# Performance work log

Measured on AMD Instinct MI355X. Metric: run time of the kernel, lower is better.

The kernel has to match this reference:

```python
import jax, jax.numpy as jnp
import numpy as np

M, N, D, P = 16, 2048, 128, 8192
H = N // D  # 16
MAXLEN = 8448
EPS = 1e-5


def layernorm(x, g, b):
    mu = jnp.mean(x, axis=-1, keepdims=True)
    var = jnp.mean(jnp.square(x - mu), axis=-1, keepdims=True)
    return (x - mu) * jax.lax.rsqrt(var + EPS) * g + b


def setup_inputs() -> dict:
    key = jax.random.key(0)
    ks = jax.random.split(key, 10)
    s = 1.0 / np.sqrt(N)  # keep activations O(1) like trained weights
    return {
        "X": jax.random.normal(ks[0], (M, N), jnp.float32),
        "ln1_g": jnp.ones((N,), jnp.float32),
        "ln1_b": jnp.zeros((N,), jnp.float32),
        "Wq": jax.random.normal(ks[1], (N, N), jnp.float32) * s,
        "Wk": jax.random.normal(ks[2], (N, N), jnp.float32) * s,
        "Wv": jax.random.normal(ks[3], (N, N), jnp.float32) * s,
        "Wo": jax.random.normal(ks[4], (N, N), jnp.float32) * s,
        "ln2_g": jnp.ones((N,), jnp.float32),
        "ln2_b": jnp.zeros((N,), jnp.float32),
        "Wup": jax.random.normal(ks[5], (4 * N, N), jnp.float32) * s,
        "Wdown": jax.random.normal(ks[6], (N, 4 * N), jnp.float32) * (1.0 / np.sqrt(4 * N)),
        "cache_K": jax.random.normal(ks[7], (H, MAXLEN, D), jnp.float32),
        "cache_V": jax.random.normal(ks[8], (H, MAXLEN, D), jnp.float32),
    }


def reference(X, ln1_g, ln1_b, Wq, Wk, Wv, Wo, ln2_g, ln2_b, Wup, Wdown, cache_K, cache_V):
    residual = X
    Xn = layernorm(X, ln1_g, ln1_b)
    # torch Linear: y = x @ W.T
    q = (Xn @ Wq.T).reshape(M, H, D).transpose(1, 0, 2)  # (H,M,D)
    k = (Xn @ Wk.T).reshape(M, H, D).transpose(1, 0, 2)
    v = (Xn @ Wv.T).reshape(M, H, D).transpose(1, 0, 2)
    # KV-cache append
    cache_K = jax.lax.dynamic_update_slice(cache_K, k, (0, P, 0))
    cache_V = jax.lax.dynamic_update_slice(cache_V, v, (0, P, 0))
    Kc = cache_K[:, : P + M, :]  # (H,T,D), T = P+M
    Vc = cache_V[:, : P + M, :]
    scores = jnp.einsum("hmd,htd->hmt", q, Kc) / np.sqrt(D)
    weights = jax.nn.softmax(scores, axis=-1)
    attn = jnp.einsum("hmt,htd->hmd", weights, Vc)  # (H,M,D)
    attn = attn.transpose(1, 0, 2).reshape(M, N)
    X = residual + attn @ Wo.T
    residual = X
    Xn = layernorm(X, ln2_g, ln2_b)
    ffn = jax.nn.gelu(Xn @ Wup.T, approximate=False) @ Wdown.T
    return residual + ffn
```

## Files before the change

### kernel.cpp

```cpp
#include <hip/hip_runtime.h>
#include <hip/hip_bf16.h>
#include <math.h>

#define M_TOK 16
#define NDIM  2048
#define DHEAD 128
#define NHEAD 16
#define MAXLEN 8448
#define FFN   8192
#define TC    64
#define NCH   129
#define LN_EPS 1e-5f
#define RSQRT_D 0.08838834764831845f

#define AS1 __attribute__((address_space(1)))
#define AS3 __attribute__((address_space(3)))

typedef float f4v __attribute__((ext_vector_type(4)));
typedef float f2v __attribute__((ext_vector_type(2)));
typedef short bf16x8 __attribute__((ext_vector_type(8)));

__device__ __forceinline__ void gload_lds16(const float* g, float* l) {
    __builtin_amdgcn_global_load_lds((AS1 void*)g, (AS3 void*)l, 16, 0, 0);
}

__device__ __forceinline__ uint32_t lds_off(const void* p) {
    return (uint32_t)(uintptr_t)(const AS3 void*)p;
}

__device__ __forceinline__ f4v dsr_b128(uint32_t off) {
    f4v r; asm volatile("ds_read_b128 %0, %1" : "=v"(r) : "v"(off)); return r;
}
__device__ __forceinline__ float dsr_b32(uint32_t off) {
    float r; asm volatile("ds_read_b32 %0, %1" : "=v"(r) : "v"(off)); return r;
}
__device__ __forceinline__ void dsw_b32(uint32_t off, float v) {
    asm volatile("ds_write_b32 %0, %1" : : "v"(off), "v"(v));
}
__device__ __forceinline__ f4v gload_b128(const float* p) {
    f4v r;
    asm volatile("global_load_dwordx4 %0, %1, off"
                 : "=v"(r) : "v"((unsigned long long)(uintptr_t)p));
    return r;
}
#define LGKM0()  asm volatile("s_waitcnt lgkmcnt(0)" ::: "memory")
#define VM0()    asm volatile("s_waitcnt vmcnt(0)" ::: "memory")
#define SCHED0() __builtin_amdgcn_sched_barrier(0)

__device__ __forceinline__ short f2bf(float x) {
    unsigned u = __float_as_uint(x);
    unsigned r = u + 0x7fffu + ((u >> 16) & 1u);
    return (short)(r >> 16);
}

template<int H>
__device__ __forceinline__ void fold_step(float* v, int lane, int o) {
    bool hi = (lane & o) != 0;
    #pragma unroll
    for (int i = 0; i < H; ++i) {
        float send = hi ? v[i] : v[i + H];
        float keep = hi ? v[i + H] : v[i];
        v[i] = keep + __shfl_xor(send, o);
    }
}

__device__ __forceinline__ void fold32(float* v, int lane) {
    fold_step<16>(v, lane, 32);
    fold_step<8>(v, lane, 16);
    fold_step<4>(v, lane, 8);
    fold_step<2>(v, lane, 4);
    fold_step<1>(v, lane, 2);
    v[0] += __shfl_xor(v[0], 1);
}

template<int KDIM>
__device__ __forceinline__ void gemv_core8(const float* __restrict__ A,
                                           const float* __restrict__ W,
                                           int cb, int w, int lane,
                                           float* sbuf, float* acc) {
    constexpr int NS = KDIM / 256;
    const float* wsrc0 = W + (size_t)(cb + 2 * w)     * KDIM + lane * 4;
    const float* wsrc1 = W + (size_t)(cb + 2 * w + 1) * KDIM + lane * 4;
    auto issue = [&](int s) {
        if (s >= NS) return;
        float* dst = sbuf + (s % 3) * 6144;
        gload_lds16(wsrc0 + s * 256, dst + (2 * w) * 256);
        gload_lds16(wsrc1 + s * 256, dst + (2 * w + 1) * 256);
        #pragma unroll
        for (int j = 0; j < 4; ++j) {
            int m = w * 4 + j;
            gload_lds16(A + (size_t)m * KDIM + s * 256 + lane * 4,
                        dst + 2048 + m * 256);
        }
    };
    issue(0); issue(1); issue(2);
    const uint32_t sb = lds_off(sbuf);
    #pragma unroll 1
    for (int s = 0; s < NS; ++s) {
        int rem = NS - 1 - s;
        if (rem >= 2)      asm volatile("s_waitcnt vmcnt(12)" ::: "memory");
        else if (rem == 1) asm volatile("s_waitcnt vmcnt(6)" ::: "memory");
        else               asm volatile("s_waitcnt vmcnt(0)" ::: "memory");
        __builtin_amdgcn_s_barrier();
        SCHED0();
        uint32_t b = sb + (uint32_t)((s % 3) * 6144) * 4u;
        f4v wr0 = dsr_b128(b + (uint32_t)((2 * w) * 256 + lane * 4) * 4u);
        f4v wr1 = dsr_b128(b + (uint32_t)((2 * w + 1) * 256 + lane * 4) * 4u);
        f4v xr[16];
        #pragma unroll
        for (int m = 0; m < 16; ++m)
            xr[m] = dsr_b128(b + (uint32_t)(2048 + m * 256 + lane * 4) * 4u);
        LGKM0();
        SCHED0();
        __builtin_amdgcn_s_barrier();
        issue(s + 3);
        #pragma unroll
        for (int m = 0; m < 16; ++m) {
            acc[m*2]   = fmaf(wr0.x, xr[m].x, acc[m*2]);
            acc[m*2]   = fmaf(wr0.y, xr[m].y, acc[m*2]);
            acc[m*2]   = fmaf(wr0.z, xr[m].z, acc[m*2]);
            acc[m*2]   = fmaf(wr0.w, xr[m].w, acc[m*2]);
            acc[m*2+1] = fmaf(wr1.x, xr[m].x, acc[m*2+1]);
            acc[m*2+1] = fmaf(wr1.y, xr[m].y, acc[m*2+1]);
            acc[m*2+1] = fmaf(wr1.z, xr[m].z, acc[m*2+1]);
            acc[m*2+1] = fmaf(wr1.w, xr[m].w, acc[m*2+1]);
        }
    }
}

__global__ __launch_bounds__(256) void k_qkv(const float* __restrict__ Xn,
                                             const float* __restrict__ Wq,
                                             const float* __restrict__ Wk,
                                             const float* __restrict__ Wv,
                                             float* __restrict__ qws,
                                             float* __restrict__ kws,
                                             float* __restrict__ vws) {
    __shared__ float sbuf[3 * 6144];
    int tid = threadIdx.x, w = tid >> 6, lane = tid & 63;
    int b = blockIdx.x;
    int sel = b >> 8;
    int cb = (b & 255) * 8;
    const float* W = (sel == 0) ? Wq : (sel == 1) ? Wk : Wv;
    float* dst = (sel == 0) ? qws : (sel == 1) ? kws : vws;
    float acc[32];
    #pragma unroll
    for (int i = 0; i < 32; ++i) acc[i] = 0.f;
    gemv_core8<2048>(Xn, W, cb, w, lane, sbuf, acc);
    fold32(acc, lane);
    if ((lane & 1) == 0) {
        int idx = (lane >> 1) & 31;
        int m = idx >> 1, c = idx & 1;
        int gcol = cb + 2 * w + c;
        int hh = gcol >> 7, d = gcol & 127;
        dst[(((size_t)hh * 16 + m) << 7) + d] = acc[0];
    }
}

__device__ __forceinline__ float gelu_exact(float x) {
    return 0.5f * x * (1.0f + erff(x * 0.7071067811865475f));
}

__global__ __launch_bounds__(256) void k_up(const float* __restrict__ A,
                                            const float* __restrict__ W,
                                            float* __restrict__ out) {
    __shared__ float sbuf[3 * 6144];
    int tid = threadIdx.x, w = tid >> 6, lane = tid & 63;
    int cb = blockIdx.x * 8;
    float acc[32];
    #pragma unroll
    for (int i = 0; i < 32; ++i) acc[i] = 0.f;
    gemv_core8<2048>(A, W, cb, w, lane, sbuf, acc);
    fold32(acc, lane);
    if ((lane & 1) == 0) {
        int idx = (lane >> 1) & 31;
        int m = idx >> 1, c = idx & 1;
        out[(size_t)m * FFN + cb + 2 * w + c] = gelu_exact(acc[0]);
    }
}

template<int KDIM>
__global__ __launch_bounds__(256) void k_resid(const float* __restrict__ A,
                                               const float* __restrict__ W,
                                               const float* __restrict__ R,
                                               float* __restrict__ out) {
    __shared__ float sbuf[3 * 6144];
    int tid = threadIdx.x, w = tid >> 6, lane = tid & 63;
    int cb = blockIdx.x * 8;
    float acc[32];
    #pragma unroll
    for (int i = 0; i < 32; ++i) acc[i] = 0.f;
    gemv_core8<KDIM>(A, W, cb, w, lane, sbuf, acc);
    fold32(acc, lane);
    if ((lane & 1) == 0) {
        int idx = (lane >> 1) & 31;
        int m = idx >> 1, c = idx & 1;
        int col = cb + 2 * w + c;
        out[(size_t)m * NDIM + col] = R[(size_t)m * NDIM + col] + acc[0];
    }
}

__global__ __launch_bounds__(256) void k_ln(const float* __restrict__ X,
                                            const float* __restrict__ g,
                                            const float* __restrict__ b,
                                            float* __restrict__ out) {
    int row = blockIdx.x, tid = threadIdx.x;
    const float4* xp = (const float4*)(X + (size_t)row * NDIM);
    float4 v0 = xp[tid], v1 = xp[tid + 256];
    float s = v0.x + v0.y + v0.z + v0.w + v1.x + v1.y + v1.z + v1.w;
    float q = v0.x*v0.x + v0.y*v0.y + v0.z*v0.z + v0.w*v0.w
            + v1.x*v1.x + v1.y*v1.y + v1.z*v1.z + v1.w*v1.w;
    #pragma unroll
    for (int o = 32; o; o >>= 1) { s += __shfl_xor(s, o); q += __shfl_xor(q, o); }
    __shared__ float ls[4], lq[4];
    int wid = tid >> 6, lane = tid & 63;
    if (lane == 0) { ls[wid] = s; lq[wid] = q; }
    __syncthreads();
    s = ls[0] + ls[1] + ls[2] + ls[3];
    q = lq[0] + lq[1] + lq[2] + lq[3];
    float mu  = s * (1.f / NDIM);
    float var = q * (1.f / NDIM) - mu * mu;
    float rs  = rsqrtf(var + LN_EPS);
    float4 g0 = ((const float4*)g)[tid], g1 = ((const float4*)g)[tid + 256];
    float4 b0 = ((const float4*)b)[tid], b1 = ((const float4*)b)[tid + 256];
    float4 o0, o1;
    o0.x = (v0.x - mu) * rs * g0.x + b0.x;  o0.y = (v0.y - mu) * rs * g0.y + b0.y;
    o0.z = (v0.z - mu) * rs * g0.z + b0.z;  o0.w = (v0.w - mu) * rs * g0.w + b0.w;
    o1.x = (v1.x - mu) * rs * g1.x + b1.x;  o1.y = (v1.y - mu) * rs * g1.y + b1.y;
    o1.z = (v1.z - mu) * rs * g1.z + b1.z;  o1.w = (v1.w - mu) * rs * g1.w + b1.w;
    float4* op = (float4*)(out + (size_t)row * NDIM);
    op[tid] = o0; op[tid + 256] = o1;
}

__global__ __launch_bounds__(256) void k_attn(const float* __restrict__ cacheK,
                                              const float* __restrict__ cacheV,
                                              const float* __restrict__ qws,
                                              const float* __restrict__ kws,
                                              const float* __restrict__ vws,
                                              float* __restrict__ part,
                                              float* __restrict__ ms) {
    __shared__ float s_k[TC * DHEAD];
    __shared__ float s_v[TC * DHEAD];
    __shared__ float s_p[16 * 68];
    int bid = blockIdx.x;
    int h = bid / NCH, c = bid % NCH;
    int nT = (c < NCH - 1) ? TC : M_TOK;
    bool full = (nT == TC);
    int nSeg = nT >> 1;
    const float* Kb = (c < NCH - 1) ? cacheK + ((size_t)h * MAXLEN + (size_t)c * TC) * DHEAD
                                    : kws + (size_t)h * M_TOK * DHEAD;
    const float* Vb = (c < NCH - 1) ? cacheV + ((size_t)h * MAXLEN + (size_t)c * TC) * DHEAD
                                    : vws + (size_t)h * M_TOK * DHEAD;
    int tid = threadIdx.x, w = tid >> 6, lane = tid & 63;
    int g = lane >> 4;

    #pragma unroll
    for (int k = 0; k < 8; ++k) {
        int j = w + 4 * k;
        if (j < nSeg) {
            int b = j * 1024 + lane * 16;
            int src = b ^ (((b >> 9) & 7) << 4);
            gload_lds16(Kb + (src >> 2), s_k + j * 256);
        }
    }

    int m_l = lane & 15;
    const float* qbase = qws + (size_t)h * M_TOK * DHEAD + (size_t)m_l * DHEAD;
    f4v qlo[4], qhi[4];
    #pragma unroll
    for (int blk = 0; blk < 4; ++blk) {
        qlo[blk] = gload_b128(qbase + blk * 32 + g * 4);
        qhi[blk] = gload_b128(qbase + blk * 32 + g * 4 + 16);
    }
    VM0();
    SCHED0();

    bf16x8 qf[4];
    #pragma unroll
    for (int blk = 0; blk < 4; ++blk) {
        qf[blk][0] = f2bf(qlo[blk].x); qf[blk][1] = f2bf(qlo[blk].y);
        qf[blk][2] = f2bf(qlo[blk].z); qf[blk][3] = f2bf(qlo[blk].w);
        qf[blk][4] = f2bf(qhi[blk].x); qf[blk][5] = f2bf(qhi[blk].y);
        qf[blk][6] = f2bf(qhi[blk].z); qf[blk][7] = f2bf(qhi[blk].w);
    }

    #pragma unroll
    for (int k = 0; k < 8; ++k) {
        int j = w + 4 * k;
        if (j < nSeg) {
            int b = j * 1024 + lane * 16;
            int src = b ^ (((b >> 9) & 7) << 4);
            gload_lds16(Vb + (src >> 2), s_v + j * 256);
        }
    }
    __builtin_amdgcn_s_barrier();

    const uint32_t skb = lds_off(s_k);
    const uint32_t svb = lds_off(s_v);
    const uint32_t spb = lds_off(s_p);

    int t0 = w * 16;
    if (t0 < nT) {
        int trow = t0 + (lane & 15);
        uint32_t xo = (uint32_t)((trow & 7) << 4);
        f4v klo[4], khi[4];
        #pragma unroll
        for (int blk = 0; blk < 4; ++blk) {
            uint32_t base = (uint32_t)(trow * 512 + blk * 128 + g * 16);
            klo[blk] = dsr_b128(skb + ((base)      ^ xo));
            khi[blk] = dsr_b128(skb + ((base + 64) ^ xo));
        }
        LGKM0();
        SCHED0();
        f4v accS = {0.f, 0.f, 0.f, 0.f};
        #pragma unroll
        for (int blk = 0; blk < 4; ++blk) {
            bf16x8 bk;
            bk[0] = f2bf(klo[blk].x); bk[1] = f2bf(klo[blk].y);
            bk[2] = f2bf(klo[blk].z); bk[3] = f2bf(klo[blk].w);
            bk[4] = f2bf(khi[blk].x); bk[5] = f2bf(khi[blk].y);
            bk[6] = f2bf(khi[blk].z); bk[7] = f2bf(khi[blk].w);
            accS = __builtin_amdgcn_mfma_f32_16x16x32_bf16(qf[blk], bk, accS, 0, 0, 0);
        }
        #pragma unroll
        for (int r = 0; r < 4; ++r) {
            int m = g * 4 + r;
            dsw_b32(spb + (uint32_t)((m * 68 + t0 + (lane & 15)) * 4), accS[r] * RSQRT_D);
        }
    }
    LGKM0();
    __builtin_amdgcn_s_barrier();

    int m2 = tid >> 4, tl = tid & 15;
    float sm_mx, sm_sum;
    {
        uint32_t prow = spb + (uint32_t)(m2 * 68 * 4);
        float r0 = dsr_b32(prow + (uint32_t)(tl * 4));
        float r1 = -1e30f, r2 = -1e30f, r3 = -1e30f;
        if (full) {
            r1 = dsr_b32(prow + (uint32_t)((tl + 16) * 4));
            r2 = dsr_b32(prow + (uint32_t)((tl + 32) * 4));
            r3 = dsr_b32(prow + (uint32_t)((tl + 48) * 4));
        }
        LGKM0();
        SCHED0();
        float mx = fmaxf(fmaxf(r0, r1), fmaxf(r2, r3));
        #pragma unroll
        for (int o = 8; o; o >>= 1) mx = fmaxf(mx, __shfl_xor(mx, o));
        float p0 = __expf(r0 - mx), sum = p0;
        dsw_b32(prow + (uint32_t)(tl * 4), p0);
        if (full) {
            float p1 = __expf(r1 - mx), p2 = __expf(r2 - mx), p3 = __expf(r3 - mx);
            sum += p1 + p2 + p3;
            dsw_b32(prow + (uint32_t)((tl + 16) * 4), p1);
            dsw_b32(prow + (uint32_t)((tl + 32) * 4), p2);
            dsw_b32(prow + (uint32_t)((tl + 48) * 4), p3);
        }
        #pragma unroll
        for (int o = 8; o; o >>= 1) sum += __shfl_xor(sum, o);
        sm_mx = mx; sm_sum = sum;
    }
    LGKM0();
    VM0();
    __builtin_amdgcn_s_barrier();

    if (!full) {
        for (int i = tid; i < 16 * 128; i += 256) {
            int r = 16 + (i >> 7), dd = i & 127;
            dsw_b32(svb + (uint32_t)((r * 512 + dd * 4) ^ ((r & 7) << 4)), 0.f);
        }
        { int m = tid >> 4, t = 16 + (tid & 15);
          dsw_b32(spb + (uint32_t)((m * 68 + t) * 4), 0.f); }
        LGKM0();
        __builtin_amdgcn_s_barrier();
    }

    f4v accO0 = {0.f,0.f,0.f,0.f}, accO1 = {0.f,0.f,0.f,0.f};
    int dc0 = w * 32 + (lane & 15);
    int nTC = (nT + 31) >> 5;
    #pragma unroll
    for (int tc = 0; tc < 2; ++tc) {
        if (tc >= nTC) break;
        int m = lane & 15;
        f4v plo = dsr_b128(spb + (uint32_t)((m * 68 + tc * 32 + g * 4) * 4));
        f4v phi = dsr_b128(spb + (uint32_t)((m * 68 + tc * 32 + g * 4 + 16) * 4));
        float va[8], vb_[8];
        #pragma unroll
        for (int half = 0; half < 2; ++half) {
            #pragma unroll
            for (int jj = 0; jj < 4; ++jj) {
                int t = tc * 32 + g * 4 + jj + half * 16;
                uint32_t xo = (uint32_t)((t & 7) << 4);
                va[half*4+jj]  = dsr_b32(svb + ((uint32_t)(t * 512 + dc0 * 4)        ^ xo));
                vb_[half*4+jj] = dsr_b32(svb + ((uint32_t)(t * 512 + (dc0+16) * 4)   ^ xo));
            }
        }
        LGKM0();
        SCHED0();
        bf16x8 pa;
        pa[0] = f2bf(plo.x); pa[1] = f2bf(plo.y); pa[2] = f2bf(plo.z); pa[3] = f2bf(plo.w);
        pa[4] = f2bf(phi.x); pa[5] = f2bf(phi.y); pa[6] = f2bf(phi.z); pa[7] = f2bf(phi.w);
        bf16x8 v0, v1;
        #pragma unroll
        for (int j = 0; j < 8; ++j) { v0[j] = f2bf(va[j]); v1[j] = f2bf(vb_[j]); }
        accO0 = __builtin_amdgcn_mfma_f32_16x16x32_bf16(pa, v0, accO0, 0, 0, 0);
        accO1 = __builtin_amdgcn_mfma_f32_16x16x32_bf16(pa, v1, accO1, 0, 0, 0);
    }

    float* pb = part + ((size_t)(h * NCH + c) * 16) * DHEAD;
    #pragma unroll
    for (int r = 0; r < 4; ++r) {
        int m = g * 4 + r;
        pb[(size_t)m * DHEAD + dc0]      = accO0[r];
        pb[(size_t)m * DHEAD + dc0 + 16] = accO1[r];
    }
    if (tl == 0) {
        float* msp = ms + ((size_t)(h * NCH + c) * 16 + m2) * 2;
        msp[0] = sm_mx; msp[1] = sm_sum;
    }
}

__global__ __launch_bounds__(256) void k_combine(const float* __restrict__ part,
                                                 const float* __restrict__ ms,
                                                 float* __restrict__ attnout) {
    __shared__ float s_scale[16][NCH + 3];
    int h = blockIdx.x >> 3, dblk = blockIdx.x & 7;
    int tid = threadIdx.x;
    {
        int cl = tid & 15, m = tid >> 4;
        float gmax = -1e30f;
        for (int c = cl; c < NCH; c += 16)
            gmax = fmaxf(gmax, ms[((size_t)(h * NCH + c) * 16 + m) * 2]);
        #pragma unroll
        for (int o = 8; o; o >>= 1) gmax = fmaxf(gmax, __shfl_xor(gmax, o));
        float denom = 0.f;
        for (int c = cl; c < NCH; c += 16) {
            const float* msp = ms + ((size_t)(h * NCH + c) * 16 + m) * 2;
            denom += msp[1] * __expf(msp[0] - gmax);
        }
        #pragma unroll
        for (int o = 8; o; o >>= 1) denom += __shfl_xor(denom, o);
        float inv = 1.f / denom;
        for (int c = cl; c < NCH; c += 16) {
            const float* msp = ms + ((size_t)(h * NCH + c) * 16 + m) * 2;
            s_scale[m][c] = __expf(msp[0] - gmax) * inv;
        }
    }
    __syncthreads();
    int m = tid >> 4, dd = tid & 15;
    int d = dblk * 16 + dd;
    const float* pp = part + ((size_t)h * NCH * 16 + m) * DHEAD + d;
    float acc = 0.f;
    #pragma unroll 4
    for (int c = 0; c < NCH; ++c)
        acc = fmaf(pp[(size_t)c * 16 * DHEAD], s_scale[m][c], acc);
    attnout[(size_t)m * NDIM + h * DHEAD + d] = acc;
}

extern "C" void kernel_launch(void* const* d_in, const int* in_sizes, int n_in,
                              void* d_out, int out_size, void* d_ws, size_t ws_size,
                              hipStream_t stream) {
    const float* X      = (const float*)d_in[0];
    const float* ln1_g  = (const float*)d_in[1];
    const float* ln1_b  = (const float*)d_in[2];
    const float* Wq     = (const float*)d_in[3];
    const float* Wk     = (const float*)d_in[4];
    const float* Wv     = (const float*)d_in[5];
    const float* Wo     = (const float*)d_in[6];
    const float* ln2_g  = (const float*)d_in[7];
    const float* ln2_b  = (const float*)d_in[8];
    const float* Wup    = (const float*)d_in[9];
    const float* Wdown  = (const float*)d_in[10];
    const float* cacheK = (const float*)d_in[11];
    const float* cacheV = (const float*)d_in[12];
    float* out = (float*)d_out;

    float* ws = (float*)d_ws;
    float* Xn1    = ws;
    float* qws    = Xn1 + 32768;
    float* kws    = qws + 32768;
    float* vws    = kws + 32768;
    float* partb  = vws + 32768;
    float* msb    = partb + 4227072;
    float* attn_o = msb + 66048;
    float* X2     = attn_o + 32768;
    float* Xn2    = X2 + 32768;
    float* ffnh   = Xn2 + 32768;

    k_ln<<<M_TOK, 256, 0, stream>>>(X, ln1_g, ln1_b, Xn1);
    k_qkv<<<768, 256, 0, stream>>>(Xn1, Wq, Wk, Wv, qws, kws, vws);
    k_attn<<<NHEAD * NCH, 256, 0, stream>>>(cacheK, cacheV, qws, kws, vws, partb, msb);
    k_combine<<<NHEAD * 8, 256, 0, stream>>>(partb, msb, attn_o);
    k_resid<2048><<<256, 256, 0, stream>>>(attn_o, Wo, X, X2);
    k_ln<<<M_TOK, 256, 0, stream>>>(X2, ln2_g, ln2_b, Xn2);
    k_up<<<1024, 256, 0, stream>>>(Xn2, Wup, ffnh);
    k_resid<8192><<<256, 256, 0, stream>>>(ffnh, Wdown, X2, out);
}
```

Before: 141.8 us.

## Replace FP32 LDS-staged GEMVs with split-K bf16 MFMA GEMMs plus epilogue kernels

```diff
diff --git a/kernel.cpp b/kernel.cpp
--- a/kernel.cpp
+++ b/kernel.cpp
@@ -23,11 +23,9 @@
 __device__ __forceinline__ void gload_lds16(const float* g, float* l) {
     __builtin_amdgcn_global_load_lds((AS1 void*)g, (AS3 void*)l, 16, 0, 0);
 }
-
 __device__ __forceinline__ uint32_t lds_off(const void* p) {
     return (uint32_t)(uintptr_t)(const AS3 void*)p;
 }
-
 __device__ __forceinline__ f4v dsr_b128(uint32_t off) {
     f4v r; asm volatile("ds_read_b128 %0, %1" : "=v"(r) : "v"(off)); return r;
 }
@@ -43,6 +41,13 @@
                  : "=v"(r) : "v"((unsigned long long)(uintptr_t)p));
     return r;
 }
+template<int OFF>
+__device__ __forceinline__ f4v gload_off(const float* p) {
+    f4v r;
+    asm volatile("global_load_dwordx4 %0, %1, off offset:%2"
+                 : "=v"(r) : "v"((unsigned long long)(uintptr_t)p), "i"(OFF));
+    return r;
+}
 #define LGKM0()  asm volatile("s_waitcnt lgkmcnt(0)" ::: "memory")
 #define VM0()    asm volatile("s_waitcnt vmcnt(0)" ::: "memory")
 #define SCHED0() __builtin_amdgcn_sched_barrier(0)
@@ -52,151 +57,130 @@
     unsigned r = u + 0x7fffu + ((u >> 16) & 1u);
     return (short)(r >> 16);
 }
-
-template<int H>
-__device__ __forceinline__ void fold_step(float* v, int lane, int o) {
-    bool hi = (lane & o) != 0;
-    #pragma unroll
-    for (int i = 0; i < H; ++i) {
-        float send = hi ? v[i] : v[i + H];
-        float keep = hi ? v[i + H] : v[i];
-        v[i] = keep + __shfl_xor(send, o);
-    }
-}
-
-__device__ __forceinline__ void fold32(float* v, int lane) {
-    fold_step<16>(v, lane, 32);
-    fold_step<8>(v, lane, 16);
-    fold_step<4>(v, lane, 8);
-    fold_step<2>(v, lane, 4);
-    fold_step<1>(v, lane, 2);
-    v[0] += __shfl_xor(v[0], 1);
-}
-
-template<int KDIM>
-__device__ __forceinline__ void gemv_core8(const float* __restrict__ A,
-                                           const float* __restrict__ W,
-                                           int cb, int w, int lane,
-                                           float* sbuf, float* acc) {
-    constexpr int NS = KDIM / 256;
-    const float* wsrc0 = W + (size_t)(cb + 2 * w)     * KDIM + lane * 4;
-    const float* wsrc1 = W + (size_t)(cb + 2 * w + 1) * KDIM + lane * 4;
-    auto issue = [&](int s) {
-        if (s >= NS) return;
-        float* dst = sbuf + (s % 3) * 6144;
-        gload_lds16(wsrc0 + s * 256, dst + (2 * w) * 256);
-        gload_lds16(wsrc1 + s * 256, dst + (2 * w + 1) * 256);
-        #pragma unroll
-        for (int j = 0; j < 4; ++j) {
-            int m = w * 4 + j;
-            gload_lds16(A + (size_t)m * KDIM + s * 256 + lane * 4,
-                        dst + 2048 + m * 256);
-        }
-    };
-    issue(0); issue(1); issue(2);
-    const uint32_t sb = lds_off(sbuf);
-    #pragma unroll 1
-    for (int s = 0; s < NS; ++s) {
-        int rem = NS - 1 - s;
-        if (rem >= 2)      asm volatile("s_waitcnt vmcnt(12)" ::: "memory");
-        else if (rem == 1) asm volatile("s_waitcnt vmcnt(6)" ::: "memory");
-        else               asm volatile("s_waitcnt vmcnt(0)" ::: "memory");
-        __builtin_amdgcn_s_barrier();
-        SCHED0();
-        uint32_t b = sb + (uint32_t)((s % 3) * 6144) * 4u;
-        f4v wr0 = dsr_b128(b + (uint32_t)((2 * w) * 256 + lane * 4) * 4u);
-        f4v wr1 = dsr_b128(b + (uint32_t)((2 * w + 1) * 256 + lane * 4) * 4u);
-        f4v xr[16];
-        #pragma unroll
-        for (int m = 0; m < 16; ++m)
-            xr[m] = dsr_b128(b + (uint32_t)(2048 + m * 256 + lane * 4) * 4u);
-        LGKM0();
-        SCHED0();
-        __builtin_amdgcn_s_barrier();
-        issue(s + 3);
-        #pragma unroll
-        for (int m = 0; m < 16; ++m) {
-            acc[m*2]   = fmaf(wr0.x, xr[m].x, acc[m*2]);
-            acc[m*2]   = fmaf(wr0.y, xr[m].y, acc[m*2]);
-            acc[m*2]   = fmaf(wr0.z, xr[m].z, acc[m*2]);
-            acc[m*2]   = fmaf(wr0.w, xr[m].w, acc[m*2]);
-            acc[m*2+1] = fmaf(wr1.x, xr[m].x, acc[m*2+1]);
-            acc[m*2+1] = fmaf(wr1.y, xr[m].y, acc[m*2+1]);
-            acc[m*2+1] = fmaf(wr1.z, xr[m].z, acc[m*2+1]);
-            acc[m*2+1] = fmaf(wr1.w, xr[m].w, acc[m*2+1]);
-        }
-    }
-}
-
-__global__ __launch_bounds__(256) void k_qkv(const float* __restrict__ Xn,
-                                             const float* __restrict__ Wq,
-                                             const float* __restrict__ Wk,
-                                             const float* __restrict__ Wv,
-                                             float* __restrict__ qws,
-                                             float* __restrict__ kws,
-                                             float* __restrict__ vws) {
-    __shared__ float sbuf[3 * 6144];
+__device__ __forceinline__ bf16x8 to8(f4v lo, f4v hi) {
+    bf16x8 r;
+    r[0]=f2bf(lo.x); r[1]=f2bf(lo.y); r[2]=f2bf(lo.z); r[3]=f2bf(lo.w);
+    r[4]=f2bf(hi.x); r[5]=f2bf(hi.y); r[6]=f2bf(hi.z); r[7]=f2bf(hi.w);
+    return r;
+}
+
+__device__ __forceinline__ f4v gemm16_512(const float* a, const float* wp) {
+    f4v acc = {0.f, 0.f, 0.f, 0.f};
+    f4v al[4][2], bl[4][2];
+#define ISSUE(c) \
+    al[(c)&3][0] = gload_off<(c)*128>(a);      \
+    al[(c)&3][1] = gload_off<(c)*128+16>(a);   \
+    bl[(c)&3][0] = gload_off<(c)*128>(wp);     \
+    bl[(c)&3][1] = gload_off<(c)*128+16>(wp);
+#define STEP(c) { \
+    if ((c) <= 12)      asm volatile("s_waitcnt vmcnt(12)" ::: "memory"); \
+    else if ((c) == 13) asm volatile("s_waitcnt vmcnt(8)"  ::: "memory"); \
+    else if ((c) == 14) asm volatile("s_waitcnt vmcnt(4)"  ::: "memory"); \
+    else                asm volatile("s_waitcnt vmcnt(0)"  ::: "memory"); \
+    SCHED0(); \
+    { bf16x8 af = to8(al[(c)&3][0], al[(c)&3][1]); \
+      bf16x8 bf = to8(bl[(c)&3][0], bl[(c)&3][1]); \
+      acc = __builtin_amdgcn_mfma_f32_16x16x32_bf16(af, bf, acc, 0, 0, 0); } \
+    if ((c) + 4 < 16) { ISSUE((c)+4) } }
+    ISSUE(0) ISSUE(1) ISSUE(2) ISSUE(3)
+    STEP(0)  STEP(1)  STEP(2)  STEP(3)
+    STEP(4)  STEP(5)  STEP(6)  STEP(7)
+    STEP(8)  STEP(9)  STEP(10) STEP(11)
+    STEP(12) STEP(13) STEP(14) STEP(15)
+#undef STEP
+#undef ISSUE
+    return acc;
+}
+
+template<int K, int N, int S>
+__global__ __launch_bounds__(256) void k_mm(const float* __restrict__ A,
+                                            const float* __restrict__ W,
+                                            float* __restrict__ part) {
+    int tid = threadIdx.x, w = tid >> 6, lane = tid & 63;
+    int nColBlk = N >> 6;
+    int colblk = blockIdx.x % nColBlk, s = blockIdx.x / nColBlk;
+    int cb = colblk * 64 + w * 16;
+    int col = cb + (lane & 15), g = lane >> 4, k0 = s * 512;
+    f4v acc = gemm16_512(A + (size_t)(lane & 15) * K + k0 + g * 8,
+                         W + (size_t)col * K + k0 + g * 8);
+    #pragma unroll
+    for (int r = 0; r < 4; ++r)
+        part[((size_t)(s * 16) + g * 4 + r) * N + col] = acc[r];
+}
+
+__global__ __launch_bounds__(256) void k_qkv_mm(const float* __restrict__ Xn,
+                                                const float* __restrict__ Wq,
+                                                const float* __restrict__ Wk,
+                                                const float* __restrict__ Wv,
+                                                float* __restrict__ pq,
+                                                float* __restrict__ pk,
+                                                float* __restrict__ pv) {
     int tid = threadIdx.x, w = tid >> 6, lane = tid & 63;
     int b = blockIdx.x;
-    int sel = b >> 8;
-    int cb = (b & 255) * 8;
+    int sel = b >> 7, bb = b & 127;
+    int colblk = bb & 31, s = bb >> 5;
     const float* W = (sel == 0) ? Wq : (sel == 1) ? Wk : Wv;
-    float* dst = (sel == 0) ? qws : (sel == 1) ? kws : vws;
-    float acc[32];
-    #pragma unroll
-    for (int i = 0; i < 32; ++i) acc[i] = 0.f;
-    gemv_core8<2048>(Xn, W, cb, w, lane, sbuf, acc);
-    fold32(acc, lane);
-    if ((lane & 1) == 0) {
-        int idx = (lane >> 1) & 31;
-        int m = idx >> 1, c = idx & 1;
-        int gcol = cb + 2 * w + c;
-        int hh = gcol >> 7, d = gcol & 127;
-        dst[(((size_t)hh * 16 + m) << 7) + d] = acc[0];
-    }
+    float* part = (sel == 0) ? pq : (sel == 1) ? pk : pv;
+    int cb = colblk * 64 + w * 16;
+    int col = cb + (lane & 15), g = lane >> 4, k0 = s * 512;
+    f4v acc = gemm16_512(Xn + (size_t)(lane & 15) * NDIM + k0 + g * 8,
+                         W + (size_t)col * NDIM + k0 + g * 8);
+    #pragma unroll
+    for (int r = 0; r < 4; ++r)
+        part[((size_t)(s * 16) + g * 4 + r) * NDIM + col] = acc[r];
 }
 
 __device__ __forceinline__ float gelu_exact(float x) {
     return 0.5f * x * (1.0f + erff(x * 0.7071067811865475f));
 }
 
-__global__ __launch_bounds__(256) void k_up(const float* __restrict__ A,
-                                            const float* __restrict__ W,
-                                            float* __restrict__ out) {
-    __shared__ float sbuf[3 * 6144];
-    int tid = threadIdx.x, w = tid >> 6, lane = tid & 63;
-    int cb = blockIdx.x * 8;
-    float acc[32];
-    #pragma unroll
-    for (int i = 0; i < 32; ++i) acc[i] = 0.f;
-    gemv_core8<2048>(A, W, cb, w, lane, sbuf, acc);
-    fold32(acc, lane);
-    if ((lane & 1) == 0) {
-        int idx = (lane >> 1) & 31;
-        int m = idx >> 1, c = idx & 1;
-        out[(size_t)m * FFN + cb + 2 * w + c] = gelu_exact(acc[0]);
-    }
-}
-
-template<int KDIM>
-__global__ __launch_bounds__(256) void k_resid(const float* __restrict__ A,
-                                               const float* __restrict__ W,
-                                               const float* __restrict__ R,
-                                               float* __restrict__ out) {
-    __shared__ float sbuf[3 * 6144];
-    int tid = threadIdx.x, w = tid >> 6, lane = tid & 63;
-    int cb = blockIdx.x * 8;
-    float acc[32];
-    #pragma unroll
-    for (int i = 0; i < 32; ++i) acc[i] = 0.f;
-    gemv_core8<KDIM>(A, W, cb, w, lane, sbuf, acc);
-    fold32(acc, lane);
-    if ((lane & 1) == 0) {
-        int idx = (lane >> 1) & 31;
-        int m = idx >> 1, c = idx & 1;
-        int col = cb + 2 * w + c;
-        out[(size_t)m * NDIM + col] = R[(size_t)m * NDIM + col] + acc[0];
-    }
+__global__ __launch_bounds__(256) void ep_qkv(const float* __restrict__ pq,
+                                              const float* __restrict__ pk,
+                                              const float* __restrict__ pv,
+                                              float* __restrict__ qws,
+                                              float* __restrict__ kws,
+                                              float* __restrict__ vws) {
+    int i = blockIdx.x * 256 + threadIdx.x;
+    int m = i >> 11, gcol = i & 2047;
+    float q = 0.f, k = 0.f, v = 0.f;
+    #pragma unroll
+    for (int s = 0; s < 4; ++s) {
+        q += pq[(size_t)s * 32768 + i];
+        k += pk[(size_t)s * 32768 + i];
+        v += pv[(size_t)s * 32768 + i];
+    }
+    int h = gcol >> 7, d = gcol & 127;
+    size_t o = (((size_t)h * 16 + m) << 7) + d;
+    qws[o] = q; kws[o] = k; vws[o] = v;
+}
+
+__global__ __launch_bounds__(256) void ep_resid4(const float* __restrict__ p,
+                                                 const float* __restrict__ R,
+                                                 float* __restrict__ out) {
+    int i = blockIdx.x * 256 + threadIdx.x;
+    float a = 0.f;
+    #pragma unroll
+    for (int s = 0; s < 4; ++s) a += p[(size_t)s * 32768 + i];
+    out[i] = R[i] + a;
+}
+
+__global__ __launch_bounds__(256) void ep_up(const float* __restrict__ p,
+                                             float* __restrict__ out) {
+    int i = blockIdx.x * 256 + threadIdx.x;
+    float a = 0.f;
+    #pragma unroll
+    for (int s = 0; s < 4; ++s) a += p[(size_t)s * 131072 + i];
+    out[i] = gelu_exact(a);
+}
+
+__global__ __launch_bounds__(256) void ep_resid16(const float* __restrict__ p,
+                                                  const float* __restrict__ R,
+                                                  float* __restrict__ out) {
+    int i = blockIdx.x * 256 + threadIdx.x;
+    float a = 0.f;
+    #pragma unroll
+    for (int s = 0; s < 16; ++s) a += p[(size_t)s * 32768 + i];
+    out[i] = R[i] + a;
 }
 
 __global__ __launch_bounds__(256) void k_ln(const float* __restrict__ X,
@@ -276,12 +260,7 @@
 
     bf16x8 qf[4];
     #pragma unroll
-    for (int blk = 0; blk < 4; ++blk) {
-        qf[blk][0] = f2bf(qlo[blk].x); qf[blk][1] = f2bf(qlo[blk].y);
-        qf[blk][2] = f2bf(qlo[blk].z); qf[blk][3] = f2bf(qlo[blk].w);
-        qf[blk][4] = f2bf(qhi[blk].x); qf[blk][5] = f2bf(qhi[blk].y);
-        qf[blk][6] = f2bf(qhi[blk].z); qf[blk][7] = f2bf(qhi[blk].w);
-    }
+    for (int blk = 0; blk < 4; ++blk) qf[blk] = to8(qlo[blk], qhi[blk]);
 
     #pragma unroll
     for (int k = 0; k < 8; ++k) {
@@ -314,11 +293,7 @@
         f4v accS = {0.f, 0.f, 0.f, 0.f};
         #pragma unroll
         for (int blk = 0; blk < 4; ++blk) {
-            bf16x8 bk;
-            bk[0] = f2bf(klo[blk].x); bk[1] = f2bf(klo[blk].y);
-            bk[2] = f2bf(klo[blk].z); bk[3] = f2bf(klo[blk].w);
-            bk[4] = f2bf(khi[blk].x); bk[5] = f2bf(khi[blk].y);
-            bk[6] = f2bf(khi[blk].z); bk[7] = f2bf(khi[blk].w);
+            bf16x8 bk = to8(klo[blk], khi[blk]);
             accS = __builtin_amdgcn_mfma_f32_16x16x32_bf16(qf[blk], bk, accS, 0, 0, 0);
         }
         #pragma unroll
@@ -390,8 +365,8 @@
             for (int jj = 0; jj < 4; ++jj) {
                 int t = tc * 32 + g * 4 + jj + half * 16;
                 uint32_t xo = (uint32_t)((t & 7) << 4);
-                va[half*4+jj]  = dsr_b32(svb + ((uint32_t)(t * 512 + dc0 * 4)        ^ xo));
-                vb_[half*4+jj] = dsr_b32(svb + ((uint32_t)(t * 512 + (dc0+16) * 4)   ^ xo));
+                va[half*4+jj]  = dsr_b32(svb + ((uint32_t)(t * 512 + dc0 * 4)      ^ xo));
+                vb_[half*4+jj] = dsr_b32(svb + ((uint32_t)(t * 512 + (dc0+16) * 4) ^ xo));
             }
         }
         LGKM0();
@@ -485,13 +460,23 @@
     float* X2     = attn_o + 32768;
     float* Xn2    = X2 + 32768;
     float* ffnh   = Xn2 + 32768;
+    float* pq     = ffnh + 131072;
+    float* pk     = pq + 131072;
+    float* pv     = pk + 131072;
+    float* po     = pv + 131072;
+    float* pu     = po + 131072;
+    float* pd     = pu + 524288;
 
     k_ln<<<M_TOK, 256, 0, stream>>>(X, ln1_g, ln1_b, Xn1);
-    k_qkv<<<768, 256, 0, stream>>>(Xn1, Wq, Wk, Wv, qws, kws, vws);
+    k_qkv_mm<<<384, 256, 0, stream>>>(Xn1, Wq, Wk, Wv, pq, pk, pv);
+    ep_qkv<<<128, 256, 0, stream>>>(pq, pk, pv, qws, kws, vws);
     k_attn<<<NHEAD * NCH, 256, 0, stream>>>(cacheK, cacheV, qws, kws, vws, partb, msb);
     k_combine<<<NHEAD * 8, 256, 0, stream>>>(partb, msb, attn_o);
-    k_resid<2048><<<256, 256, 0, stream>>>(attn_o, Wo, X, X2);
+    k_mm<2048, 2048, 4><<<128, 256, 0, stream>>>(attn_o, Wo, po);
+    ep_resid4<<<128, 256, 0, stream>>>(po, X, X2);
     k_ln<<<M_TOK, 256, 0, stream>>>(X2, ln2_g, ln2_b, Xn2);
-    k_up<<<1024, 256, 0, stream>>>(Xn2, Wup, ffnh);
-    k_resid<8192><<<256, 256, 0, stream>>>(ffnh, Wdown, X2, out);
-}
+    k_mm<2048, 8192, 4><<<512, 256, 0, stream>>>(Xn2, Wup, pu);
+    ep_up<<<512, 256, 0, stream>>>(pu, ffnh);
+    k_mm<8192, 2048, 16><<<512, 256, 0, stream>>>(ffnh, Wdown, pd);
+    ep_resid16<<<128, 256, 0, stream>>>(pd, X2, out);
+}
```

Measured after the change: 138.9 us. -2.0%, faster.
